# Kernel tuning notes

Hardware: AMD Instinct MI355X
Metric: run time of the kernel (lower is better)

The kernel has to match this reference:

```python
import jax, jax.numpy as jnp
import numpy as np

G_DCN = 32   # DCNv2 conv groups
KSZ = 3      # kernel size
P = KSZ * KSZ  # 9 sampling points
G_POST = 256  # post 1x1 conv groups
C_OUT = 2048


def _dcnv2(x, w_off, b_off, w_dcn, b_dcn):
    """Modulated deformable conv v2 (stride 1, pad 1, deformable_groups=1)."""
    B, C, H, W = x.shape
    # offset/mask branch: 3x3 conv -> 27 channels = (dy[9], dx[9], mask[9])
    off = jax.lax.conv_general_dilated(
        x, w_off, (1, 1), ((1, 1), (1, 1)),
        dimension_numbers=('NCHW', 'OIHW', 'NCHW')) + b_off[None, :, None, None]
    dy, dx = off[:, :P], off[:, P:2 * P]
    m = jax.nn.sigmoid(off[:, 2 * P:])            # [B,P,H,W] modulation mask
    ky = (jnp.arange(P) // KSZ - 1).astype(x.dtype)  # kernel row offsets -1,0,1
    kx = (jnp.arange(P) % KSZ - 1).astype(x.dtype)
    hh = jnp.arange(H, dtype=x.dtype)[None, None, :, None]
    ww = jnp.arange(W, dtype=x.dtype)[None, None, None, :]
    sy = hh + ky[None, :, None, None] + dy        # [B,P,H,W] sample rows
    sx = ww + kx[None, :, None, None] + dx        # [B,P,H,W] sample cols
    y0f = jnp.floor(sy); x0f = jnp.floor(sx)
    wy = sy - y0f; wx = sx - x0f
    y0 = y0f.astype(jnp.int32); x0 = x0f.astype(jnp.int32)
    flat = x.reshape(B, C, H * W)

    def corner(yi, xi):
        ok = ((yi >= 0) & (yi < H) & (xi >= 0) & (xi < W)).astype(x.dtype)
        idx = (jnp.clip(yi, 0, H - 1) * W + jnp.clip(xi, 0, W - 1)).reshape(B, -1)
        v = jax.vmap(lambda f, i: f[:, i])(flat, idx).reshape(B, C, P, H, W)
        return v * ok[:, None]

    val = (corner(y0, x0) * ((1 - wy) * (1 - wx))[:, None]
           + corner(y0, x0 + 1) * ((1 - wy) * wx)[:, None]
           + corner(y0 + 1, x0) * (wy * (1 - wx))[:, None]
           + corner(y0 + 1, x0 + 1) * (wy * wx)[:, None])
    val = val * m[:, None]                        # [B,C,P,H,W]
    in_pg = C // G_DCN
    out_pg = w_dcn.shape[0] // G_DCN
    xs = val.reshape(B, G_DCN, in_pg, P, H, W)
    ws = w_dcn.reshape(G_DCN, out_pg, in_pg, P)
    out = jnp.einsum('bgiphw,goip->bgohw', xs, ws).reshape(B, -1, H, W)
    return out + b_dcn[None, :, None, None]


def setup_inputs() -> dict:
    key = jax.random.key(0)
    ks = jax.random.split(key, 8)
    lo_res = jax.random.normal(ks[0], (2, 2048, 32, 32), dtype=jnp.float32)
    hi_res = jax.random.normal(ks[1], (2, 1024, 64, 64), dtype=jnp.float32)
    # offset conv weights kept small so sampled locations stay near the grid
    w_off = jax.random.normal(ks[2], (27, 1024, 3, 3), dtype=jnp.float32) * 0.01
    b_off = jnp.zeros((27,), dtype=jnp.float32)
    w_dcn = jax.random.normal(ks[3], (1024, 32, 3, 3), dtype=jnp.float32) * (1.0 / np.sqrt(32 * 9))
    b_dcn = jax.random.normal(ks[4], (1024,), dtype=jnp.float32) * 0.01
    w_post = jax.random.normal(ks[5], (2048, 12), dtype=jnp.float32) * (1.0 / np.sqrt(12))
    b_post = jax.random.normal(ks[6], (2048,), dtype=jnp.float32) * 0.01
    return {"lo_res": lo_res, "hi_res": hi_res, "w_off": w_off, "b_off": b_off,
            "w_dcn": w_dcn, "b_dcn": b_dcn, "w_post": w_post, "b_post": b_post}


def reference(lo_res, hi_res, w_off, b_off, w_dcn, b_dcn, w_post, b_post):
    B, Clo, h, w = lo_res.shape
    # policy=0: bilinear x2 upsample (align_corners=False == half-pixel, jax default)
    lo_up = jax.image.resize(lo_res, (B, Clo, 2 * h, 2 * w), method='bilinear')
    hi_al = _dcnv2(hi_res, w_off, b_off, w_dcn, b_dcn)
    x = jnp.concatenate([lo_up, hi_al], axis=1)   # [B,3072,H,W]
    H, W = x.shape[2], x.shape[3]
    in_pg = x.shape[1] // G_POST                  # 12
    out_pg = C_OUT // G_POST                      # 8
    xs = x.reshape(B, G_POST, in_pg, H, W)
    ws = w_post.reshape(G_POST, out_pg, in_pg)
    out = jnp.einsum('bgihw,goi->bgohw', xs, ws).reshape(B, C_OUT, H, W)
    return out + b_post[None, :, None, None]
```

## Files before the change

### kernel.cpp

```cpp
#include <hip/hip_runtime.h>
#include <hip/hip_fp16.h>
#include <cstdint>

static constexpr size_t OFF_XT   = 0;
static constexpr size_t OFF_HIAL = 16777216;
static constexpr size_t OFF_PART = OFF_HIAL;
static constexpr size_t OFF_MU   = OFF_HIAL + 33554432;
static constexpr size_t OFF_WA   = OFF_MU  + 2ull*9*4096*16;
static constexpr size_t OFF_WB   = OFF_WA  + 36864ull*16;

using f16x8 = __attribute__((ext_vector_type(8))) _Float16;
typedef __attribute__((ext_vector_type(4))) float f32x4;
typedef __attribute__((ext_vector_type(2))) float f32x2;

__device__ __forceinline__ uint16_t f2h(float f) { return __half_as_ushort(__float2half(f)); }
__device__ __forceinline__ __half2 u2h(uint32_t u) { union { uint32_t u; __half2 h; } x; x.u = u; return x.h; }
__device__ __forceinline__ uint32_t h2u(__half2 h) { union { uint32_t u; __half2 h; } x; x.h = h; return x.u; }

__device__ __forceinline__ f16x8 blend4h(uint4 A, uint4 B, uint4 C, uint4 D,
                                         __half2 wab, __half2 wcd) {
    __half2 h00 = __half2half2(__low2half(wab));
    __half2 h01 = __half2half2(__high2half(wab));
    __half2 h10 = __half2half2(__low2half(wcd));
    __half2 h11 = __half2half2(__high2half(wcd));
    const uint32_t* a = (const uint32_t*)&A;
    const uint32_t* b = (const uint32_t*)&B;
    const uint32_t* c = (const uint32_t*)&C;
    const uint32_t* d = (const uint32_t*)&D;
    union { uint32_t u[4]; f16x8 v; } r;
#pragma unroll
    for (int e = 0; e < 4; ++e) {
        __half2 acc = __hmul2(h00, u2h(a[e]));
        acc = __hfma2(h01, u2h(b[e]), acc);
        acc = __hfma2(h10, u2h(c[e]), acc);
        acc = __hfma2(h11, u2h(d[e]), acc);
        r.u[e] = h2u(acc);
    }
    return r.v;
}

__global__ void k_prep(const float* __restrict__ w_off, const float* __restrict__ w_dcn,
                       uint4* __restrict__ waT, uint32_t* __restrict__ wb) {
    int idx = blockIdx.x * 256 + threadIdx.x;
    if (idx < 36864) {
        int kg = idx & 3, col = (idx >> 2) & 15, mt = (idx >> 6) & 1;
        int ks = (idx >> 7) & 3, kc = (idx >> 9) & 7, p = idx >> 12;
        int oc = mt * 16 + col;
        int chb = kc * 128 + ks * 32 + kg * 8;
        union { uint32_t u[4]; uint4 v; } r;
#pragma unroll
        for (int e = 0; e < 4; ++e) {
            uint32_t lo = 0, hi = 0;
            if (oc < 27) {
                lo = f2h(w_off[(size_t)oc * 9216 + (size_t)(chb + 2 * e) * 9 + p]);
                hi = f2h(w_off[(size_t)oc * 9216 + (size_t)(chb + 2 * e + 1) * 9 + p]);
            }
            r.u[e] = lo | (hi << 16);
        }
        waT[idx] = r.v;
    } else {
        int j = idx - 36864;
        if (j >= 32 * 9 * 32 * 16) return;
        int g = j / (9 * 32 * 16), r = j % (9 * 32 * 16);
        int p = r / (32 * 16), r2 = r % (32 * 16), o = r2 / 16, ip = r2 % 16;
        uint32_t lo = f2h(w_dcn[((size_t)(g * 32 + o) * 32 + 2 * ip) * 9 + p]);
        uint32_t hi = f2h(w_dcn[((size_t)(g * 32 + o) * 32 + 2 * ip + 1) * 9 + p]);
        wb[j] = lo | (hi << 16);
    }
}

__global__ void k_transpose(const float* __restrict__ x, uint32_t* __restrict__ xt) {
    __shared__ float tile[64][65];
    int cblk = blockIdx.x * 64, y = blockIdx.y, b = blockIdx.z, t = threadIdx.x;
    const float* src = x + ((size_t)(b * 1024 + cblk)) * 4096 + y * 64;
#pragma unroll
    for (int k = 0; k < 16; ++k) {
        int lin = t + k * 256;
        int cl = lin >> 6, xx = lin & 63;
        tile[cl][xx] = src[(size_t)cl * 4096 + xx];
    }
    __syncthreads();
    int kc = cblk >> 7, half = (cblk & 64) >> 1;
    uint32_t* dst = xt + ((size_t)(b * 8 + kc) * 4096 + (size_t)y * 64) * 64 + half;
#pragma unroll
    for (int k = 0; k < 8; ++k) {
        int lin = t + k * 256;
        int xx = lin >> 5, cp = lin & 31;
        uint32_t lo = f2h(tile[2 * cp][xx]);
        uint32_t hi = f2h(tile[2 * cp + 1][xx]);
        dst[(size_t)xx * 64 + cp] = lo | (hi << 16);
    }
}

__global__ __launch_bounds__(256, 4) void k_offconv_mfma(const uint32_t* __restrict__ xt,
                                                         const uint4* __restrict__ waT,
                                                         __half* __restrict__ part) {
    __shared__ uint4 sb[1632];
    int bx = blockIdx.x;
    int y = bx >> 1, xh = bx & 1;
    int kc = blockIdx.y, b = blockIdx.z;
    int t = threadIdx.x, wave = t >> 6, lane = t & 63;
    int pxg = wave >> 1, mt = wave & 1;
    int col = lane & 15, kg = lane >> 4;

    {
        const uint32_t* srcb = xt + ((size_t)(b * 8 + kc) * 4096) * 64;
#pragma unroll
        for (int i = 0; i < 7; ++i) {
            int idx = i * 256 + t;
            if (idx < 1632) {
                int s = idx >> 4, q = idx & 15;
                int rr = s >= 68 ? 2 : (s >= 34 ? 1 : 0);
                int pxl = s - rr * 34;
                int gy = y - 1 + rr, gx = xh * 32 - 1 + pxl;
                uint4 val = uint4{0, 0, 0, 0};
                if (gy >= 0 && gy < 64 && gx >= 0 && gx < 64)
                    val = *(const uint4*)(srcb + ((size_t)(gy * 64 + gx)) * 64 + q * 4);
                sb[s * 16 + (q ^ (s & 15))] = val;
            }
        }
    }
    __syncthreads();

    f32x4 acc[9];
#pragma unroll
    for (int p = 0; p < 9; ++p) acc[p] = f32x4{0.f, 0.f, 0.f, 0.f};

#pragma unroll
    for (int p = 0; p < 9; ++p) {
        int ky = p / 3 - 1, kx = p % 3 - 1;
        int pxl = pxg * 16 + col + kx + 1;
        int s = (ky + 1) * 34 + pxl;
#pragma unroll
        for (int ks = 0; ks < 4; ++ks) {
            f16x8 bfr = *(const f16x8*)&sb[s * 16 + ((ks * 4 + kg) ^ (s & 15))];
            int gidx = ((((p * 8 + kc) * 4 + ks) * 2 + mt) * 16 + col) * 4 + kg;
            f16x8 afr = *(const f16x8*)&waT[gidx];
            acc[p] = __builtin_amdgcn_mfma_f32_16x16x32_f16(afr, bfr, acc[p], 0, 0, 0);
        }
    }

    int px = y * 64 + xh * 32 + pxg * 16 + col;
    int ocl = mt * 16 + kg * 4;
#pragma unroll
    for (int p = 0; p < 9; ++p) {
        __half* pc = part + ((size_t)((kc * 9 + p) * 2 + b)) * 28 * 4096 + px;
#pragma unroll
        for (int j = 0; j < 4; ++j)
            if (ocl + j < 28) pc[(size_t)(ocl + j) * 4096] = __float2half(acc[p][j]);
    }
}

__global__ void k_meta(const __half* __restrict__ part, const float* __restrict__ b_off,
                       uint4* __restrict__ mu) {
    int idx = blockIdx.x * 256 + threadIdx.x;
    if (idx >= 2 * 9 * 4096) return;
    int b = idx / (9 * 4096), r = idx % (9 * 4096), p = r / 4096, hw = r % 4096;
    int h = hw >> 6, w = hw & 63;
    float sdy = b_off[p], sdx = b_off[p + 9], sm = b_off[p + 18];
#pragma unroll 4
    for (int s = 0; s < 72; ++s) {
        const __half* pb = part + ((size_t)(s * 2 + b)) * 28 * 4096 + hw;
        sdy += __half2float(pb[(size_t)p * 4096]);
        sdx += __half2float(pb[(size_t)(p + 9) * 4096]);
        sm  += __half2float(pb[(size_t)(p + 18) * 4096]);
    }
    float m = 1.f / (1.f + expf(-sm));
    int ky = p / 3 - 1, kx = p % 3 - 1;
    float sy = (float)(h + ky) + sdy;
    float sx = (float)(w + kx) + sdx;
    float y0f = floorf(sy), x0f = floorf(sx);
    float wy = sy - y0f, wx = sx - x0f;
    int y0 = (int)fminf(fmaxf(y0f, -2.f), 64.f);
    int x0 = (int)fminf(fmaxf(x0f, -2.f), 64.f);
    bool vy0 = (y0 >= 0) && (y0 < 64), vy1 = (y0 + 1 >= 0) && (y0 + 1 < 64);
    bool vx0 = (x0 >= 0) && (x0 < 64), vx1 = (x0 + 1 >= 0) && (x0 + 1 < 64);
    float w00 = (1.f - wy) * (1.f - wx) * m * ((vy0 && vx0) ? 1.f : 0.f);
    float w01 = (1.f - wy) * wx         * m * ((vy0 && vx1) ? 1.f : 0.f);
    float w10 = wy * (1.f - wx)         * m * ((vy1 && vx0) ? 1.f : 0.f);
    float w11 = wy * wx                 * m * ((vy1 && vx1) ? 1.f : 0.f);
    int cy0 = min(max(y0, 0), 63),     cx0 = min(max(x0, 0), 63);
    int cy1 = min(max(y0 + 1, 0), 63), cx1 = min(max(x0 + 1, 0), 63);
    int blo = (h >> 3) * 8 - 6;
    blo = blo < 0 ? 0 : (blo > 44 ? 44 : blo);
    int blo64 = blo * 64;
    int s0 = cy0 * 64 + cx0 - blo64, s1 = cy0 * 64 + cx1 - blo64;
    int s2 = cy1 * 64 + cx0 - blo64, s3 = cy1 * 64 + cx1 - blo64;
    uint32_t wlo = (uint32_t)f2h(w00) | ((uint32_t)f2h(w01) << 16);
    uint32_t whi = (uint32_t)f2h(w10) | ((uint32_t)f2h(w11) << 16);
    uint32_t ilo = ((uint32_t)(uint16_t)(short)s0) | (((uint32_t)(uint16_t)(short)s1) << 16);
    uint32_t ihi = ((uint32_t)(uint16_t)(short)s2) | (((uint32_t)(uint16_t)(short)s3) << 16);
    mu[idx] = uint4{wlo, whi, ilo, ihi};
}

__global__ __launch_bounds__(512, 4) void k_dcn_lds(const uint32_t* __restrict__ xt,
                                                    const uint32_t* __restrict__ wb,
                                                    const uint4* __restrict__ mu,
                                                    const float* __restrict__ b_dcn,
                                                    float* __restrict__ hial) {
    __shared__ uint4 ldsq[5120];
    int g = blockIdx.x, band = blockIdx.y, b = blockIdx.z;
    int y0 = band * 8;
    int band_lo = y0 - 6;
    if (band_lo < 0) band_lo = 0;
    if (band_lo > 44) band_lo = 44;
    int t = threadIdx.x;

    {
        const uint32_t* src = xt + ((size_t)(b * 8 + (g >> 2)) * 4096 + (size_t)band_lo * 64) * 64 + (g & 3) * 16;
#pragma unroll
        for (int i = 0; i < 10; ++i) {
            int Q = i * 512 + t;
            int s = Q >> 2;
            int q = (Q & 3) ^ ((s >> 1) & 3);
            ldsq[Q] = *(const uint4*)(src + (size_t)s * 64 + q * 4);
        }
    }
    __syncthreads();
    const uint32_t* ldsb = (const uint32_t*)ldsq;

    int wave = t >> 6, lane = t & 63;
    int col = lane & 15, kg = lane >> 4;
    int strip = (wave & 3) * 16;
    int rbase = (wave >> 2) * 4;
    const uint32_t* xb = xt + ((size_t)(b * 8 + (g >> 2)) * 4096) * 64 + (g & 3) * 16 + kg * 4;
    const uint32_t* wg = wb + (size_t)g * 9 * 32 * 16 + col * 16 + kg * 4;
    const uint4* mub = mu + (size_t)b * 9 * 4096;
    const float* bd  = b_dcn + g * 32;
    int blo64 = band_lo * 64;

#define LDSRD(SS) (*(const uint4*)(ldsb + (SS) * 16 + ((kg ^ (((SS) >> 1) & 3)) << 2)))
#define GSLOW(SS, U)                                                               \
    {                                                                              \
        int s_ = (SS);                                                             \
        int sc_ = s_ < 0 ? 0 : (s_ > 1279 ? 1279 : s_);                            \
        U = LDSRD(sc_);                                                            \
        if ((unsigned)s_ >= 1280u)                                                 \
            U = *(const uint4*)(xb + (size_t)(s_ + blo64) * 64);                   \
    }

    for (int r = 0; r < 4; ++r) {
        int pix = (y0 + rbase + r) * 64 + strip + col;
        f32x4 acc0 = {0.f, 0.f, 0.f, 0.f};
        f32x4 acc1 = {0.f, 0.f, 0.f, 0.f};
#pragma unroll
        for (int p = 0; p < 9; ++p) {
            uint4 cm = mub[p * 4096 + pix];
            int s0 = (short)(cm.z & 0xffffu), s1 = (short)(cm.z >> 16);
            int s2 = (short)(cm.w & 0xffffu), s3 = (short)(cm.w >> 16);
            unsigned mx = (unsigned)s0;
            mx = mx > (unsigned)s1 ? mx : (unsigned)s1;
            mx = mx > (unsigned)s2 ? mx : (unsigned)s2;
            mx = mx > (unsigned)s3 ? mx : (unsigned)s3;
            uint4 u0, u1, u2, u3;
            if (__builtin_expect(mx >= 1280u, 0)) {
                GSLOW(s0, u0)
                GSLOW(s1, u1)
                GSLOW(s2, u2)
                GSLOW(s3, u3)
            } else {
                u0 = LDSRD(s0);
                u1 = LDSRD(s1);
                u2 = LDSRD(s2);
                u3 = LDSRD(s3);
            }
            f16x8 bfr = blend4h(u0, u1, u2, u3, u2h(cm.x), u2h(cm.y));
            const uint32_t* ap = wg + (size_t)p * 512;
            f16x8 af0 = *(const f16x8*)ap;
            f16x8 af1 = *(const f16x8*)(ap + 256);
            acc0 = __builtin_amdgcn_mfma_f32_16x16x32_f16(af0, bfr, acc0, 0, 0, 0);
            acc1 = __builtin_amdgcn_mfma_f32_16x16x32_f16(af1, bfr, acc1, 0, 0, 0);
        }
        float* pc = hial + ((size_t)b * 1024 + g * 32) * 4096 + pix;
#pragma unroll
        for (int j = 0; j < 4; ++j) {
            pc[(size_t)(kg * 4 + j) * 4096]      = acc0[j] + bd[kg * 4 + j];
            pc[(size_t)(16 + kg * 4 + j) * 4096] = acc1[j] + bd[16 + kg * 4 + j];
        }
    }
#undef LDSRD
#undef GSLOW
}

__global__ __launch_bounds__(256, 4) void k_post5(const float* __restrict__ lo,
                                                  const float* __restrict__ hial,
                                                  const float* __restrict__ wp,
                                                  const float* __restrict__ bp,
                                                  float* __restrict__ out) {
    int gq = blockIdx.x, kq = blockIdx.y, b = blockIdx.z;
    int t = threadIdx.x;
    int g = __builtin_amdgcn_readfirstlane(gq * 4 + (t >> 6));
    int lane = t & 63, k = kq * 4 + (lane >> 4), w4 = lane & 15;
    int rm = k > 0 ? k - 1 : 0, rp = k < 31 ? k + 1 : 31;
    int lc = 2 * w4 - 1; lc = lc < 0 ? 0 : (lc > 28 ? 28 : lc);
    bool is0 = (w4 == 0), is15 = (w4 == 15);

    f32x4 acc0[8], acc1[8];
#pragma unroll
    for (int o = 0; o < 8; ++o) {
        float bv = bp[g * 8 + o];
        acc0[o] = f32x4{bv, bv, bv, bv};
        acc1[o] = acc0[o];
    }
    const float* wrow = wp + (size_t)g * 96;
    int cbase = g * 12;

#define UPROW(LB, R, H)                                                            \
    {                                                                              \
        f32x4 q = *(const f32x4*)((LB) + (R) * 32 + lc);                           \
        float e0 = is15 ? q.y : q.x;                                               \
        float p0 = is0 ? q.x : (is15 ? q.z : q.y);                                 \
        float p1 = is0 ? q.y : (is15 ? q.w : q.z);                                 \
        float e3 = is0 ? q.z : q.w;                                                \
        H = f32x4{0.25f * e0 + 0.75f * p0, 0.75f * p0 + 0.25f * p1,                \
                  0.25f * p0 + 0.75f * p1, 0.75f * p1 + 0.25f * e3};               \
    }
#define LOCH(I)                                                                    \
    {                                                                              \
        const float* lb = lo + ((size_t)(b * 2048 + cbase + (I))) * 1024;          \
        f32x4 hm, hk, hp;                                                          \
        UPROW(lb, rm, hm) UPROW(lb, k, hk) UPROW(lb, rp, hp)                       \
        f32x4 va = 0.25f * hm + 0.75f * hk;                                        \
        f32x4 vb = 0.75f * hk + 0.25f * hp;                                        \
        _Pragma("unroll")                                                          \
        for (int o = 0; o < 8; ++o) {                                              \
            float w = wrow[o * 12 + (I)];                                          \
            acc0[o] += w * va;                                                     \
            acc1[o] += w * vb;                                                     \
        }                                                                          \
    }
#define HICH(I)                                                                    \
    {                                                                              \
        const float* hb = hial + ((size_t)(b * 1024 + cbase + (I) - 2048)) * 4096  \
                          + (size_t)(2 * k) * 64 + 4 * w4;                         \
        f32x4 va = *(const f32x4*)hb;                                              \
        f32x4 vb = *(const f32x4*)(hb + 64);                                       \
        _Pragma("unroll")                                                          \
        for (int o = 0; o < 8; ++o) {                                              \
            float w = wrow[o * 12 + (I)];                                          \
            acc0[o] += w * va;                                                     \
            acc1[o] += w * vb;                                                     \
        }                                                                          \
    }

    if (g <= 169) {
#pragma unroll 4
        for (int i = 0; i < 12; ++i) LOCH(i)
    } else if (g >= 171) {
#pragma unroll 4
        for (int i = 0; i < 12; ++i) HICH(i)
    } else {
#pragma unroll 4
        for (int i = 0; i < 8; ++i) LOCH(i)
#pragma unroll
        for (int i = 8; i < 12; ++i) HICH(i)
    }
#undef LOCH
#undef HICH
#undef UPROW

    float* ob = out + ((size_t)(b * 2048 + g * 8)) * 4096 + (size_t)(2 * k) * 64 + 4 * w4;
#pragma unroll
    for (int o = 0; o < 8; ++o) {
        __builtin_nontemporal_store(acc0[o], (f32x4*)(ob + (size_t)o * 4096));
        __builtin_nontemporal_store(acc1[o], (f32x4*)(ob + (size_t)o * 4096 + 64));
    }
}

extern "C" void kernel_launch(void* const* d_in, const int* in_sizes, int n_in,
                              void* d_out, int out_size, void* d_ws, size_t ws_size,
                              hipStream_t stream) {
    const float* lo_res = (const float*)d_in[0];
    const float* hi_res = (const float*)d_in[1];
    const float* w_off  = (const float*)d_in[2];
    const float* b_off  = (const float*)d_in[3];
    const float* w_dcn  = (const float*)d_in[4];
    const float* b_dcn  = (const float*)d_in[5];
    const float* w_post = (const float*)d_in[6];
    const float* b_post = (const float*)d_in[7];
    float* out = (float*)d_out;
    char* ws = (char*)d_ws;

    uint32_t* xt  = (uint32_t*)(ws + OFF_XT);
    float* hial   = (float*)(ws + OFF_HIAL);
    __half* part  = (__half*)(ws + OFF_PART);
    uint4* mup    = (uint4*)(ws + OFF_MU);
    uint4* waT    = (uint4*)(ws + OFF_WA);
    uint32_t* wbp = (uint32_t*)(ws + OFF_WB);

    k_prep<<<(36864 + 32 * 9 * 32 * 16 + 255) / 256, 256, 0, stream>>>(w_off, w_dcn, waT, wbp);
    k_transpose<<<dim3(16, 64, 2), 256, 0, stream>>>(hi_res, xt);
    k_offconv_mfma<<<dim3(128, 8, 2), 256, 0, stream>>>(xt, waT, part);
    k_meta<<<(2 * 9 * 4096 + 255) / 256, 256, 0, stream>>>(part, b_off, mup);
    k_dcn_lds<<<dim3(32, 8, 2), 512, 0, stream>>>(xt, wbp, mup, b_dcn, hial);
    k_post5<<<dim3(64, 8, 2), 256, 0, stream>>>(lo_res, hial, w_post, b_post, out);
}
```

Baseline: 113.0 us.

## Halve offset-conv partials via two-chunk register-staged loop; store DCN output as fp16

```diff
diff --git a/kernel.cpp b/kernel.cpp
--- a/kernel.cpp
+++ b/kernel.cpp
@@ -98,53 +98,76 @@
     __shared__ uint4 sb[1632];
     int bx = blockIdx.x;
     int y = bx >> 1, xh = bx & 1;
-    int kc = blockIdx.y, b = blockIdx.z;
+    int kh = blockIdx.y, b = blockIdx.z;
     int t = threadIdx.x, wave = t >> 6, lane = t & 63;
     int pxg = wave >> 1, mt = wave & 1;
     int col = lane & 15, kg = lane >> 4;
 
-    {
-        const uint32_t* srcb = xt + ((size_t)(b * 8 + kc) * 4096) * 64;
-#pragma unroll
-        for (int i = 0; i < 7; ++i) {
-            int idx = i * 256 + t;
-            if (idx < 1632) {
-                int s = idx >> 4, q = idx & 15;
-                int rr = s >= 68 ? 2 : (s >= 34 ? 1 : 0);
-                int pxl = s - rr * 34;
-                int gy = y - 1 + rr, gx = xh * 32 - 1 + pxl;
-                uint4 val = uint4{0, 0, 0, 0};
-                if (gy >= 0 && gy < 64 && gx >= 0 && gx < 64)
-                    val = *(const uint4*)(srcb + ((size_t)(gy * 64 + gx)) * 64 + q * 4);
-                sb[s * 16 + (q ^ (s & 15))] = val;
+    f32x4 acc[9];
+#pragma unroll
+    for (int p = 0; p < 9; ++p) acc[p] = f32x4{0.f, 0.f, 0.f, 0.f};
+
+    uint4 stg[7];
+#define STAGE_LOAD(KC)                                                             \
+    {                                                                              \
+        const uint32_t* srcb = xt + ((size_t)(b * 8 + (KC)) * 4096) * 64;          \
+        _Pragma("unroll")                                                          \
+        for (int i = 0; i < 7; ++i) {                                              \
+            int idx = i * 256 + t;                                                 \
+            stg[i] = uint4{0, 0, 0, 0};                                            \
+            if (idx < 1632) {                                                      \
+                int s = idx >> 4, q = idx & 15;                                    \
+                int rr = s >= 68 ? 2 : (s >= 34 ? 1 : 0);                          \
+                int pxl = s - rr * 34;                                             \
+                int gy = y - 1 + rr, gx = xh * 32 - 1 + pxl;                       \
+                if (gy >= 0 && gy < 64 && gx >= 0 && gx < 64)                      \
+                    stg[i] = *(const uint4*)(srcb + ((size_t)(gy * 64 + gx)) * 64 + q * 4); \
+            }                                                                      \
+        }                                                                          \
+    }
+#define STAGE_WRITE                                                                \
+    {                                                                              \
+        _Pragma("unroll")                                                          \
+        for (int i = 0; i < 7; ++i) {                                              \
+            int idx = i * 256 + t;                                                 \
+            if (idx < 1632) {                                                      \
+                int s = idx >> 4, q = idx & 15;                                    \
+                sb[s * 16 + (q ^ (s & 15))] = stg[i];                              \
+            }                                                                      \
+        }                                                                          \
+    }
+
+    int kc0 = kh * 2;
+    STAGE_LOAD(kc0)
+#pragma unroll
+    for (int c2 = 0; c2 < 2; ++c2) {
+        int kc = kc0 + c2;
+        STAGE_WRITE
+        __syncthreads();
+        if (c2 == 0) STAGE_LOAD(kc0 + 1)
+#pragma unroll
+        for (int p = 0; p < 9; ++p) {
+            int ky = p / 3 - 1, kx = p % 3 - 1;
+            int pxl = pxg * 16 + col + kx + 1;
+            int s = (ky + 1) * 34 + pxl;
+#pragma unroll
+            for (int ks = 0; ks < 4; ++ks) {
+                f16x8 bfr = *(const f16x8*)&sb[s * 16 + ((ks * 4 + kg) ^ (s & 15))];
+                int gidx = ((((p * 8 + kc) * 4 + ks) * 2 + mt) * 16 + col) * 4 + kg;
+                f16x8 afr = *(const f16x8*)&waT[gidx];
+                acc[p] = __builtin_amdgcn_mfma_f32_16x16x32_f16(afr, bfr, acc[p], 0, 0, 0);
             }
         }
-    }
-    __syncthreads();
-
-    f32x4 acc[9];
-#pragma unroll
-    for (int p = 0; p < 9; ++p) acc[p] = f32x4{0.f, 0.f, 0.f, 0.f};
-
-#pragma unroll
-    for (int p = 0; p < 9; ++p) {
-        int ky = p / 3 - 1, kx = p % 3 - 1;
-        int pxl = pxg * 16 + col + kx + 1;
-        int s = (ky + 1) * 34 + pxl;
-#pragma unroll
-        for (int ks = 0; ks < 4; ++ks) {
-            f16x8 bfr = *(const f16x8*)&sb[s * 16 + ((ks * 4 + kg) ^ (s & 15))];
-            int gidx = ((((p * 8 + kc) * 4 + ks) * 2 + mt) * 16 + col) * 4 + kg;
-            f16x8 afr = *(const f16x8*)&waT[gidx];
-            acc[p] = __builtin_amdgcn_mfma_f32_16x16x32_f16(afr, bfr, acc[p], 0, 0, 0);
-        }
-    }
+        __syncthreads();
+    }
+#undef STAGE_LOAD
+#undef STAGE_WRITE
 
     int px = y * 64 + xh * 32 + pxg * 16 + col;
     int ocl = mt * 16 + kg * 4;
 #pragma unroll
     for (int p = 0; p < 9; ++p) {
-        __half* pc = part + ((size_t)((kc * 9 + p) * 2 + b)) * 28 * 4096 + px;
+        __half* pc = part + ((size_t)((kh * 9 + p) * 2 + b)) * 28 * 4096 + px;
 #pragma unroll
         for (int j = 0; j < 4; ++j)
             if (ocl + j < 28) pc[(size_t)(ocl + j) * 4096] = __float2half(acc[p][j]);
@@ -159,7 +182,7 @@
     int h = hw >> 6, w = hw & 63;
     float sdy = b_off[p], sdx = b_off[p + 9], sm = b_off[p + 18];
 #pragma unroll 4
-    for (int s = 0; s < 72; ++s) {
+    for (int s = 0; s < 36; ++s) {
         const __half* pb = part + ((size_t)(s * 2 + b)) * 28 * 4096 + hw;
         sdy += __half2float(pb[(size_t)p * 4096]);
         sdx += __half2float(pb[(size_t)(p + 9) * 4096]);
@@ -197,7 +220,7 @@
                                                     const uint32_t* __restrict__ wb,
                                                     const uint4* __restrict__ mu,
                                                     const float* __restrict__ b_dcn,
-                                                    float* __restrict__ hial) {
+                                                    __half* __restrict__ hial) {
     __shared__ uint4 ldsq[5120];
     int g = blockIdx.x, band = blockIdx.y, b = blockIdx.z;
     int y0 = band * 8;
@@ -271,11 +294,11 @@
             acc0 = __builtin_amdgcn_mfma_f32_16x16x32_f16(af0, bfr, acc0, 0, 0, 0);
             acc1 = __builtin_amdgcn_mfma_f32_16x16x32_f16(af1, bfr, acc1, 0, 0, 0);
         }
-        float* pc = hial + ((size_t)b * 1024 + g * 32) * 4096 + pix;
+        __half* pc = hial + ((size_t)b * 1024 + g * 32) * 4096 + pix;
 #pragma unroll
         for (int j = 0; j < 4; ++j) {
-            pc[(size_t)(kg * 4 + j) * 4096]      = acc0[j] + bd[kg * 4 + j];
-            pc[(size_t)(16 + kg * 4 + j) * 4096] = acc1[j] + bd[16 + kg * 4 + j];
+            pc[(size_t)(kg * 4 + j) * 4096]      = __float2half(acc0[j] + bd[kg * 4 + j]);
+            pc[(size_t)(16 + kg * 4 + j) * 4096] = __float2half(acc1[j] + bd[16 + kg * 4 + j]);
         }
     }
 #undef LDSRD
@@ -283,7 +306,7 @@
 }
 
 __global__ __launch_bounds__(256, 4) void k_post5(const float* __restrict__ lo,
-                                                  const float* __restrict__ hial,
+                                                  const __half* __restrict__ hial,
                                                   const float* __restrict__ wp,
                                                   const float* __restrict__ bp,
                                                   float* __restrict__ out) {
@@ -331,10 +354,16 @@
     }
 #define HICH(I)                                                                    \
     {                                                                              \
-        const float* hb = hial + ((size_t)(b * 1024 + cbase + (I) - 2048)) * 4096  \
+        const __half* hb = hial + ((size_t)(b * 1024 + cbase + (I) - 2048)) * 4096 \
                           + (size_t)(2 * k) * 64 + 4 * w4;                         \
-        f32x4 va = *(const f32x4*)hb;                                              \
-        f32x4 vb = *(const f32x4*)(hb + 64);                                       \
+        __half2 ha0 = *(const __half2*)(hb);                                       \
+        __half2 ha1 = *(const __half2*)(hb + 2);                                   \
+        __half2 hb0 = *(const __half2*)(hb + 64);                                  \
+        __half2 hb1 = *(const __half2*)(hb + 66);                                  \
+        f32x4 va = {__half2float(ha0.x), __half2float(ha0.y),                      \
+                    __half2float(ha1.x), __half2float(ha1.y)};                     \
+        f32x4 vb = {__half2float(hb0.x), __half2float(hb0.y),                      \
+                    __half2float(hb1.x), __half2float(hb1.y)};                     \
         _Pragma("unroll")                                                          \
         for (int o = 0; o < 8; ++o) {                                              \
             float w = wrow[o * 12 + (I)];                                          \
@@ -382,7 +411,7 @@
     char* ws = (char*)d_ws;
 
     uint32_t* xt  = (uint32_t*)(ws + OFF_XT);
-    float* hial   = (float*)(ws + OFF_HIAL);
+    __half* hial  = (__half*)(ws + OFF_HIAL);
     __half* part  = (__half*)(ws + OFF_PART);
     uint4* mup    = (uint4*)(ws + OFF_MU);
     uint4* waT    = (uint4*)(ws + OFF_WA);
@@ -390,7 +419,7 @@
 
     k_prep<<<(36864 + 32 * 9 * 32 * 16 + 255) / 256, 256, 0, stream>>>(w_off, w_dcn, waT, wbp);
     k_transpose<<<dim3(16, 64, 2), 256, 0, stream>>>(hi_res, xt);
-    k_offconv_mfma<<<dim3(128, 8, 2), 256, 0, stream>>>(xt, waT, part);
+    k_offconv_mfma<<<dim3(128, 4, 2), 256, 0, stream>>>(xt, waT, part);
     k_meta<<<(2 * 9 * 4096 + 255) / 256, 256, 0, stream>>>(part, b_off, mup);
     k_dcn_lds<<<dim3(32, 8, 2), 512, 0, stream>>>(xt, wbp, mup, b_dcn, hial);
     k_post5<<<dim3(64, 8, 2), 256, 0, stream>>>(lo_res, hial, w_post, b_post, out);
```

Measured after the change: 105.8 us. 6.4% less time.
